# Kernel tuning notes

Hardware: AMD Instinct MI355X
Metric: run time of the kernel (lower is better)

The kernel has to match this reference:

```python
import jax, jax.numpy as jnp
import numpy as np


def setup_inputs() -> dict:
    T, B, D = 2048, 8, 1024
    key = jax.random.key(0)
    k1, k2, k3 = jax.random.split(key, 3)
    # xavier-uniform-ish scale for [D, D] weights
    lim = float(np.sqrt(6.0 / (D + D)))
    return {
        "x": jax.random.normal(k1, (T, B, D), dtype=jnp.float32),
        "h0": jnp.zeros((B, D), dtype=jnp.float32),
        "W_alpha": jax.random.uniform(k2, (D, D), dtype=jnp.float32, minval=-lim, maxval=lim),
        "b_alpha": jnp.full((D,), 2.0, dtype=jnp.float32),  # init_alpha_bias
        "W_x": jax.random.uniform(k3, (D, D), dtype=jnp.float32, minval=-lim, maxval=lim),
        "b": jnp.zeros((D,), dtype=jnp.float32),
    }


def reference(x, h0, W_alpha, b_alpha, W_x, b):
    # Precompute input projections for all timesteps (one big GEMM each).
    # alpha_t = sigmoid(W_alpha @ x_t + b_alpha); v_t = tanh(h_{t-1} + W_x @ x_t + b)
    alpha_all = jax.nn.sigmoid(jnp.einsum('tbd,ed->tbe', x, W_alpha) + b_alpha)  # [T,B,D]
    wx_all = jnp.einsum('tbd,ed->tbe', x, W_x) + b                                # [T,B,D]

    def step(h_prev, inp):
        alpha, wx = inp
        v = jnp.tanh(h_prev + wx)
        h_new = alpha * h_prev + (1.0 - alpha) * v
        out = h_new * jax.nn.silu(h_new)
        return h_new, (out, h_new)

    _, (output, hs) = jax.lax.scan(step, h0, (alpha_all, wx_all))
    h = jnp.concatenate([h0[None], hs], axis=0)  # [T+1, B, D]
    return output, h
```

## Files before the change

### kernel.cpp

```cpp
#include <hip/hip_runtime.h>
#include <hip/hip_bf16.h>
#include <cstdint>
#include <cstddef>

#define T_STEPS 2048
#define BATCH   8
#define D_DIM   1024
#define M_ROWS  (T_STEPS * BATCH)
#define N_COLS  (2 * D_DIM)
#define K_DIM   D_DIM
#define NCH     (BATCH * D_DIM)

#define BM 128
#define BN 128
#define BK 32

typedef __bf16 bf16x8 __attribute__((ext_vector_type(8)));
typedef float  f32x4  __attribute__((ext_vector_type(4)));

__device__ __forceinline__ unsigned short f2bf_rne(float f) {
    union { float f; unsigned u; } c; c.f = f;
    unsigned u = c.u;
    u += 0x7fffu + ((u >> 16) & 1u);
    return (unsigned short)(u >> 16);
}

__device__ __forceinline__ float sigmoid_f(float z) {
    return 1.0f / (1.0f + __expf(-z));
}

__device__ __forceinline__ void glds16(const void* gptr, void* lptr) {
    __builtin_amdgcn_global_load_lds(
        (const __attribute__((address_space(1))) unsigned int*)gptr,
        (__attribute__((address_space(3))) unsigned int*)lptr,
        16, 0, 0);
}

__global__ void cvt_bf16_kernel(const float* __restrict__ src,
                                unsigned short* __restrict__ dst, int n4) {
    int i = blockIdx.x * blockDim.x + threadIdx.x;
    if (i >= n4) return;
    float4 v = reinterpret_cast<const float4*>(src)[i];
    ushort4 o;
    o.x = f2bf_rne(v.x); o.y = f2bf_rne(v.y);
    o.z = f2bf_rne(v.z); o.w = f2bf_rne(v.w);
    reinterpret_cast<ushort4*>(dst)[i] = o;
}

__global__ __launch_bounds__(256, 2)
void gemm_kernel(const unsigned short* __restrict__ A,
                 const unsigned short* __restrict__ Bm,
                 const float* __restrict__ b_alpha,
                 const float* __restrict__ b_x,
                 float* __restrict__ alpha_out,
                 float* __restrict__ wx_out)
{
    __shared__ unsigned short sA[BM * BK];
    __shared__ unsigned short sB[BN * BK];

    const int tid  = threadIdx.x;
    const int wave = tid >> 6;
    const int lane = tid & 63;

    const int orig = blockIdx.y * 16 + blockIdx.x;
    const int swz  = (orig & 7) * 256 + (orig >> 3);
    const int rowBase = (swz >> 4) * BM;
    const int colBase = (swz & 15) * BN;

    const int wr = (wave >> 1) * 64;
    const int wc = (wave & 1) * 64;

    const int laneHi = lane >> 4;
    const int laneLo = lane & 15;

    const int dRow = lane >> 2;
    const int dCol = (lane & 3) * 8;

    f32x4 acc[4][4];
#pragma unroll
    for (int i = 0; i < 4; i++)
#pragma unroll
        for (int j = 0; j < 4; j++)
            acc[i][j] = (f32x4)(0.0f);

    for (int k0 = 0; k0 < K_DIM; k0 += BK) {
#pragma unroll
        for (int p = 0; p < 2; ++p) {
            const int seg = wave * 2 + p;
            glds16(A + (size_t)(rowBase + seg * 16 + dRow) * K_DIM + k0 + dCol,
                   &sA[seg * 512]);
            glds16(Bm + (size_t)(colBase + seg * 16 + dRow) * K_DIM + k0 + dCol,
                   &sB[seg * 512]);
        }
        __syncthreads();

        bf16x8 af[4], bfr[4];
#pragma unroll
        for (int i = 0; i < 4; i++)
            af[i] = *reinterpret_cast<const bf16x8*>(
                &sA[(wr + i * 16 + laneLo) * BK + laneHi * 8]);
#pragma unroll
        for (int j = 0; j < 4; j++)
            bfr[j] = *reinterpret_cast<const bf16x8*>(
                &sB[(wc + j * 16 + laneLo) * BK + laneHi * 8]);
        __syncthreads();

#pragma unroll
        for (int i = 0; i < 4; i++)
#pragma unroll
            for (int j = 0; j < 4; j++)
                acc[i][j] = __builtin_amdgcn_mfma_f32_16x16x32_bf16(
                    af[i], bfr[j], acc[i][j], 0, 0, 0);
    }

#pragma unroll
    for (int i = 0; i < 4; i++) {
        int row = rowBase + wr + i * 16 + laneHi * 4;
#pragma unroll
        for (int j = 0; j < 4; j++) {
            int col = colBase + wc + j * 16 + laneLo;
            if (col < D_DIM) {
                float bias = b_alpha[col];
#pragma unroll
                for (int r = 0; r < 4; r++) {
                    float z = acc[i][j][r] + bias;
                    alpha_out[(size_t)(row + r) * D_DIM + col] = sigmoid_f(z);
                }
            } else {
                int c2 = col - D_DIM;
                float bias = b_x[c2];
#pragma unroll
                for (int r = 0; r < 4; r++)
                    wx_out[(size_t)(row + r) * D_DIM + c2] = acc[i][j][r] + bias;
            }
        }
    }
}

#define TT   32
#define NT   (T_STEPS / TT)
#define PF   6
#define CPB  32
#define SHS  36

__global__ __launch_bounds__(192)
void scan_kernel(const float* __restrict__ alpha,
                 const float* __restrict__ wx,
                 const float* __restrict__ h0,
                 float* __restrict__ out,
                 float* __restrict__ hout)
{
    __shared__ float sIn[8][2][TT * CPB];
    __shared__ float sH[2][TT * SHS];

    const int lane = threadIdx.x & 63;
    const int wid  = threadIdx.x >> 6;
    const int ch0  = blockIdx.x * CPB;

    const float C2L = 2.88539008177792681472f;

    const int q8 = lane >> 3;
    const int c4 = (lane & 7) * 4;

    float h = 0.0f;

    if (wid == 1) {
#pragma unroll
        for (int t = 0; t < PF; ++t)
#pragma unroll
            for (int p = 0; p < TT / 8; ++p) {
                const size_t g = (size_t)(t * TT + p * 8 + q8) * NCH + ch0 + c4;
                glds16(alpha + g, &sIn[t][0][p * 256]);
                glds16(wx    + g, &sIn[t][1][p * 256]);
            }
        asm volatile("s_waitcnt vmcnt(40)" ::: "memory");
    } else if (wid == 0) {
        if (lane < CPB) h = h0[ch0 + lane];
    } else {
        if (lane < CPB) hout[ch0 + lane] = h0[ch0 + lane];
    }
    __builtin_amdgcn_s_barrier();
    __builtin_amdgcn_sched_barrier(0);

    for (int tile = 0; tile < NT; ++tile) {
        if (wid == 0) {
            const float* sA  = &sIn[tile & 7][0][0];
            const float* sW  = &sIn[tile & 7][1][0];
            float* sHc       = &sH[tile & 1][0];
            if (lane < CPB) {
#pragma unroll 8
                for (int ts = 0; ts < TT; ++ts) {
                    const float a = sA[ts * CPB + lane];
                    const float w = sW[ts * CPB + lane];
                    const float u = 1.0f - a;
                    const float p = (h + w) * C2L;
                    const float e = __builtin_amdgcn_exp2f(p);
                    const float r = __builtin_amdgcn_rcpf(e + 1.0f);
                    const float m = fmaf(a, h, u);
                    h = fmaf(-(u + u), r, m);
                    sHc[ts * SHS + lane] = h;
                }
            }
            asm volatile("s_waitcnt lgkmcnt(0)" ::: "memory");
            __builtin_amdgcn_sched_barrier(0);
        } else if (wid == 1) {
            if (tile + PF < NT) {
                const int b  = (tile + PF) & 7;
                const int t0 = (tile + PF) * TT;
#pragma unroll
                for (int p = 0; p < TT / 8; ++p) {
                    const size_t g = (size_t)(t0 + p * 8 + q8) * NCH + ch0 + c4;
                    glds16(alpha + g, &sIn[b][0][p * 256]);
                    glds16(wx    + g, &sIn[b][1][p * 256]);
                }
            }
            {
                const int rem = NT - 1 - tile;
                if (rem >= PF) {
                    asm volatile("s_waitcnt vmcnt(40)" ::: "memory");
                } else if (rem == 5) {
                    asm volatile("s_waitcnt vmcnt(32)" ::: "memory");
                } else if (rem == 4) {
                    asm volatile("s_waitcnt vmcnt(24)" ::: "memory");
                } else if (rem == 3) {
                    asm volatile("s_waitcnt vmcnt(16)" ::: "memory");
                } else if (rem == 2) {
                    asm volatile("s_waitcnt vmcnt(8)" ::: "memory");
                } else if (rem == 1) {
                    asm volatile("s_waitcnt vmcnt(0)" ::: "memory");
                }
            }
            __builtin_amdgcn_sched_barrier(0);
        } else {
            if (tile >= 1) {
                const float* sHs = &sH[(tile - 1) & 1][0];
                const int tb = (tile - 1) * TT;
#pragma unroll
                for (int i = 0; i < TT / 8; ++i) {
                    const int tsrow = i * 8 + q8;
                    const float4 hv = *reinterpret_cast<const float4*>(
                        &sHs[tsrow * SHS + c4]);
                    *reinterpret_cast<float4*>(
                        &hout[(size_t)(tb + tsrow + 1) * NCH + ch0 + c4]) = hv;
                    float4 o;
                    o.x = hv.x * hv.x * sigmoid_f(hv.x);
                    o.y = hv.y * hv.y * sigmoid_f(hv.y);
                    o.z = hv.z * hv.z * sigmoid_f(hv.z);
                    o.w = hv.w * hv.w * sigmoid_f(hv.w);
                    *reinterpret_cast<float4*>(
                        &out[(size_t)(tb + tsrow) * NCH + ch0 + c4]) = o;
                }
            }
        }
        __builtin_amdgcn_s_barrier();
        __builtin_amdgcn_sched_barrier(0);
    }

    if (wid == 2) {
        const float* sHs = &sH[(NT - 1) & 1][0];
        const int tb = (NT - 1) * TT;
#pragma unroll
        for (int i = 0; i < TT / 8; ++i) {
            const int tsrow = i * 8 + q8;
            const float4 hv = *reinterpret_cast<const float4*>(
                &sHs[tsrow * SHS + c4]);
            *reinterpret_cast<float4*>(
                &hout[(size_t)(tb + tsrow + 1) * NCH + ch0 + c4]) = hv;
            float4 o;
            o.x = hv.x * hv.x * sigmoid_f(hv.x);
            o.y = hv.y * hv.y * sigmoid_f(hv.y);
            o.z = hv.z * hv.z * sigmoid_f(hv.z);
            o.w = hv.w * hv.w * sigmoid_f(hv.w);
            *reinterpret_cast<float4*>(
                &out[(size_t)(tb + tsrow) * NCH + ch0 + c4]) = o;
        }
    }
}

extern "C" void kernel_launch(void* const* d_in, const int* in_sizes, int n_in,
                              void* d_out, int out_size, void* d_ws, size_t ws_size,
                              hipStream_t stream) {
    const float* x       = (const float*)d_in[0];
    const float* h0      = (const float*)d_in[1];
    const float* W_alpha = (const float*)d_in[2];
    const float* b_alpha = (const float*)d_in[3];
    const float* W_x     = (const float*)d_in[4];
    const float* b       = (const float*)d_in[5];

    float* out  = (float*)d_out;
    float* hout = out + (size_t)T_STEPS * BATCH * D_DIM;

    float* ws_alpha = (float*)d_ws;
    float* ws_wx    = ws_alpha + (size_t)M_ROWS * D_DIM;
    unsigned short* ws_x = (unsigned short*)(ws_wx + (size_t)M_ROWS * D_DIM);
    unsigned short* ws_W = ws_x + (size_t)M_ROWS * K_DIM;

    {
        int n4 = M_ROWS * K_DIM / 4;
        cvt_bf16_kernel<<<(n4 + 255) / 256, 256, 0, stream>>>(x, ws_x, n4);
    }
    {
        int n4 = D_DIM * K_DIM / 4;
        cvt_bf16_kernel<<<(n4 + 255) / 256, 256, 0, stream>>>(W_alpha, ws_W, n4);
        cvt_bf16_kernel<<<(n4 + 255) / 256, 256, 0, stream>>>(
            W_x, ws_W + (size_t)D_DIM * K_DIM, n4);
    }

    {
        dim3 grid(N_COLS / BN, M_ROWS / BM);
        gemm_kernel<<<grid, 256, 0, stream>>>(ws_x, ws_W, b_alpha, b,
                                              ws_alpha, ws_wx);
    }

    scan_kernel<<<NCH / CPB, 192, 0, stream>>>(ws_alpha, ws_wx, h0, out, hout);
}
```

Measured before the change: 360.8 us.

## Double GEMM K-tile with XOR-swizzled LDS and shorten scan recurrence critical path

```diff
diff --git a/kernel.cpp b/kernel.cpp
--- a/kernel.cpp
+++ b/kernel.cpp
@@ -13,7 +13,7 @@
 
 #define BM 128
 #define BN 128
-#define BK 32
+#define BK 64
 
 typedef __bf16 bf16x8 __attribute__((ext_vector_type(8)));
 typedef float  f32x4  __attribute__((ext_vector_type(4)));
@@ -72,9 +72,10 @@
 
     const int laneHi = lane >> 4;
     const int laneLo = lane & 15;
-
-    const int dRow = lane >> 2;
-    const int dCol = (lane & 3) * 8;
+    const int rxor   = laneLo & 7;
+
+    const int dRow   = lane >> 3;
+    const int dColSw = ((lane & 7) ^ dRow) * 8;
 
     f32x4 acc[4][4];
 #pragma unroll
@@ -85,32 +86,38 @@
 
     for (int k0 = 0; k0 < K_DIM; k0 += BK) {
 #pragma unroll
-        for (int p = 0; p < 2; ++p) {
-            const int seg = wave * 2 + p;
-            glds16(A + (size_t)(rowBase + seg * 16 + dRow) * K_DIM + k0 + dCol,
+        for (int p = 0; p < 4; ++p) {
+            const int seg = wave * 4 + p;
+            glds16(A + (size_t)(rowBase + seg * 8 + dRow) * K_DIM + k0 + dColSw,
                    &sA[seg * 512]);
-            glds16(Bm + (size_t)(colBase + seg * 16 + dRow) * K_DIM + k0 + dCol,
+            glds16(Bm + (size_t)(colBase + seg * 8 + dRow) * K_DIM + k0 + dColSw,
                    &sB[seg * 512]);
         }
         __syncthreads();
 
-        bf16x8 af[4], bfr[4];
-#pragma unroll
-        for (int i = 0; i < 4; i++)
-            af[i] = *reinterpret_cast<const bf16x8*>(
-                &sA[(wr + i * 16 + laneLo) * BK + laneHi * 8]);
-#pragma unroll
-        for (int j = 0; j < 4; j++)
-            bfr[j] = *reinterpret_cast<const bf16x8*>(
-                &sB[(wc + j * 16 + laneLo) * BK + laneHi * 8]);
+#pragma unroll
+        for (int kk = 0; kk < 2; ++kk) {
+            bf16x8 af[4], bfr[4];
+#pragma unroll
+            for (int i = 0; i < 4; i++) {
+                const int row = wr + i * 16 + laneLo;
+                af[i] = *reinterpret_cast<const bf16x8*>(
+                    &sA[row * BK + (((kk << 2) + laneHi) ^ rxor) * 8]);
+            }
+#pragma unroll
+            for (int j = 0; j < 4; j++) {
+                const int row = wc + j * 16 + laneLo;
+                bfr[j] = *reinterpret_cast<const bf16x8*>(
+                    &sB[row * BK + (((kk << 2) + laneHi) ^ rxor) * 8]);
+            }
+#pragma unroll
+            for (int i = 0; i < 4; i++)
+#pragma unroll
+                for (int j = 0; j < 4; j++)
+                    acc[i][j] = __builtin_amdgcn_mfma_f32_16x16x32_bf16(
+                        af[i], bfr[j], acc[i][j], 0, 0, 0);
+        }
         __syncthreads();
-
-#pragma unroll
-        for (int i = 0; i < 4; i++)
-#pragma unroll
-            for (int j = 0; j < 4; j++)
-                acc[i][j] = __builtin_amdgcn_mfma_f32_16x16x32_bf16(
-                    af[i], bfr[j], acc[i][j], 0, 0, 0);
     }
 
 #pragma unroll
@@ -188,16 +195,21 @@
             const float* sW  = &sIn[tile & 7][1][0];
             float* sHc       = &sH[tile & 1][0];
             if (lane < CPB) {
-#pragma unroll 8
+                float zl = (h + sW[lane]) * C2L;
+#pragma unroll
                 for (int ts = 0; ts < TT; ++ts) {
-                    const float a = sA[ts * CPB + lane];
-                    const float w = sW[ts * CPB + lane];
-                    const float u = 1.0f - a;
-                    const float p = (h + w) * C2L;
-                    const float e = __builtin_amdgcn_exp2f(p);
-                    const float r = __builtin_amdgcn_rcpf(e + 1.0f);
-                    const float m = fmaf(a, h, u);
-                    h = fmaf(-(u + u), r, m);
+                    const float a   = sA[ts * CPB + lane];
+                    const float e   = __builtin_amdgcn_exp2f(zl);
+                    const float u   = 1.0f - a;
+                    const float n2u = -(u + u);
+                    const float m   = fmaf(a, h, u);
+                    const float r   = __builtin_amdgcn_rcpf(e + 1.0f);
+                    if (ts < TT - 1) {
+                        const float cwn = sW[(ts + 1) * CPB + lane] * C2L;
+                        const float K   = fmaf(m, C2L, cwn);
+                        zl = fmaf(n2u * C2L, r, K);
+                    }
+                    h = fmaf(n2u, r, m);
                     sHc[ts * SHS + lane] = h;
                 }
             }
```

After: 347.6 us. 3.7% less time.
